# Optimization experiments

Measured on AMD Instinct MI355X. Metric: run time of the kernel, lower is better.

Reference implementation:

```python
import jax, jax.numpy as jnp
import numpy as np

D = 64          # node_hidden_dim
MP_STEPS = 6    # num_step_message_passing
S2S_STEPS = 6   # num_step_set2set
LSTM_LAYERS = 3 # num_layer_set2set


def setup_inputs() -> dict:
    key = jax.random.key(0)
    ks = jax.random.split(key, 32)
    N, E, B = 10000, 50000, 500
    node_in, edge_in, edge_hid, out_dim = 15, 5, 128, 12
    s = 0.1
    inp = {}
    inp["node_feat"] = jax.random.normal(ks[0], (N, node_in), jnp.float32)
    inp["edge_feat"] = jax.random.normal(ks[1], (E, edge_in), jnp.float32)
    inp["src"] = jax.random.randint(ks[2], (E,), 0, N)
    inp["dst"] = jax.random.randint(ks[3], (E,), 0, N)
    inp["graph_ids"] = jnp.sort(jax.random.randint(ks[4], (N,), 0, B))
    inp["num_graphs"] = B
    # lin0
    inp["lin0_W"] = jax.random.normal(ks[5], (node_in, D), jnp.float32) * s
    inp["lin0_b"] = jnp.zeros((D,), jnp.float32)
    # edge network MLP (Linear -> ReLU -> Linear), output reshaped to D x D per edge
    inp["em_W1"] = jax.random.normal(ks[6], (edge_in, edge_hid), jnp.float32) * s
    inp["em_b1"] = jnp.zeros((edge_hid,), jnp.float32)
    inp["em_W2"] = jax.random.normal(ks[7], (edge_hid, D * D), jnp.float32) * 0.02
    inp["em_b2"] = jnp.zeros((D * D,), jnp.float32)
    inp["conv_bias"] = jnp.zeros((D,), jnp.float32)
    # GRU (input D, hidden D), torch layout: [3*D, in], gate order r,z,n
    inp["gru_Wih"] = jax.random.normal(ks[8], (3 * D, D), jnp.float32) * s
    inp["gru_Whh"] = jax.random.normal(ks[9], (3 * D, D), jnp.float32) * s
    inp["gru_bih"] = jnp.zeros((3 * D,), jnp.float32)
    inp["gru_bhh"] = jnp.zeros((3 * D,), jnp.float32)
    # Set2Set LSTM: input 2*D, hidden D, 3 layers. torch layout [4*D, in], gates i,f,g,o
    inp["lstm0_Wih"] = jax.random.normal(ks[10], (4 * D, 2 * D), jnp.float32) * s
    inp["lstm0_Whh"] = jax.random.normal(ks[11], (4 * D, D), jnp.float32) * s
    inp["lstm0_bih"] = jnp.zeros((4 * D,), jnp.float32)
    inp["lstm0_bhh"] = jnp.zeros((4 * D,), jnp.float32)
    inp["lstm12_Wih"] = jax.random.normal(ks[12], (2, 4 * D, D), jnp.float32) * s
    inp["lstm12_Whh"] = jax.random.normal(ks[13], (2, 4 * D, D), jnp.float32) * s
    inp["lstm12_bih"] = jnp.zeros((2, 4 * D), jnp.float32)
    inp["lstm12_bhh"] = jnp.zeros((2, 4 * D), jnp.float32)
    # output head
    inp["lin1_W"] = jax.random.normal(ks[14], (2 * D, D), jnp.float32) * s
    inp["lin1_b"] = jnp.zeros((D,), jnp.float32)
    inp["lin2_W"] = jax.random.normal(ks[15], (D, out_dim), jnp.float32) * s
    inp["lin2_b"] = jnp.zeros((out_dim,), jnp.float32)
    return inp


def _mpnn(node_feat, edge_feat, src, dst, graph_ids, num_graphs,
          lin0_W, lin0_b, em_W1, em_b1, em_W2, em_b2, conv_bias,
          gru_Wih, gru_Whh, gru_bih, gru_bhh,
          lstm0_Wih, lstm0_Whh, lstm0_bih, lstm0_bhh,
          lstm12_Wih, lstm12_Whh, lstm12_bih, lstm12_bhh,
          lin1_W, lin1_b, lin2_W, lin2_b):
    N = node_feat.shape[0]
    E = edge_feat.shape[0]
    B = num_graphs
    # initial node embedding
    out = jax.nn.relu(node_feat @ lin0_W + lin0_b)      # [N, D]
    h = out                                             # GRU hidden (seq_len=1, 1 layer)
    # per-edge weight matrices (edge features are static across steps)
    We = (jax.nn.relu(edge_feat @ em_W1 + em_b1) @ em_W2 + em_b2).reshape(E, D, D)
    for _ in range(MP_STEPS):
        # NNConv: gather src -> per-edge matvec -> scatter-add to dst
        msg = jnp.einsum('ei,eio->eo', out[src], We)    # [E, D]
        agg = jax.ops.segment_sum(msg, dst, num_segments=N) + conv_bias
        m = jax.nn.relu(agg)                            # [N, D]
        # GRU cell (torch gate order r, z, n)
        gx = m @ gru_Wih.T + gru_bih
        gh = h @ gru_Whh.T + gru_bhh
        rx, zx, nx = jnp.split(gx, 3, axis=-1)
        rh, zh, nh = jnp.split(gh, 3, axis=-1)
        r = jax.nn.sigmoid(rx + rh)
        z = jax.nn.sigmoid(zx + zh)
        n = jnp.tanh(nx + r * nh)
        h = (1.0 - z) * n + z * h
        out = h
    # Set2Set readout: 3-layer LSTM over steps, attention over nodes per graph
    h_l = [jnp.zeros((B, D), out.dtype) for _ in range(LSTM_LAYERS)]
    c_l = [jnp.zeros((B, D), out.dtype) for _ in range(LSTM_LAYERS)]
    q_star = jnp.zeros((B, 2 * D), out.dtype)
    for _ in range(S2S_STEPS):
        x = q_star
        for l in range(LSTM_LAYERS):
            if l == 0:
                Wih, Whh, bih, bhh = lstm0_Wih, lstm0_Whh, lstm0_bih, lstm0_bhh
            else:
                Wih, Whh = lstm12_Wih[l - 1], lstm12_Whh[l - 1]
                bih, bhh = lstm12_bih[l - 1], lstm12_bhh[l - 1]
            g = x @ Wih.T + bih + h_l[l] @ Whh.T + bhh
            i_g, f_g, g_g, o_g = jnp.split(g, 4, axis=-1)
            c_l[l] = jax.nn.sigmoid(f_g) * c_l[l] + jax.nn.sigmoid(i_g) * jnp.tanh(g_g)
            h_l[l] = jax.nn.sigmoid(o_g) * jnp.tanh(c_l[l])
            x = h_l[l]
        q = x                                           # [B, D]
        # segment softmax attention
        e = jnp.sum(out * q[graph_ids], axis=-1)        # [N]
        emax = jax.ops.segment_max(e, graph_ids, num_segments=B)
        ex = jnp.exp(e - emax[graph_ids])
        denom = jax.ops.segment_sum(ex, graph_ids, num_segments=B)
        alpha = ex / denom[graph_ids]                   # [N]
        readout = jax.ops.segment_sum(alpha[:, None] * out, graph_ids, num_segments=B)
        q_star = jnp.concatenate([q, readout], axis=-1) # [B, 2D]
    y = jax.nn.relu(q_star @ lin1_W + lin1_b) @ lin2_W + lin2_b
    return y


def reference(node_feat, edge_feat, src, dst, graph_ids, num_graphs,
              lin0_W, lin0_b, em_W1, em_b1, em_W2, em_b2, conv_bias,
              gru_Wih, gru_Whh, gru_bih, gru_bhh,
              lstm0_Wih, lstm0_Whh, lstm0_bih, lstm0_bhh,
              lstm12_Wih, lstm12_Whh, lstm12_bih, lstm12_bhh,
              lin1_W, lin1_b, lin2_W, lin2_b):
    return _mpnn(node_feat, edge_feat, src, dst, graph_ids, num_graphs,
                 lin0_W, lin0_b, em_W1, em_b1, em_W2, em_b2, conv_bias,
                 gru_Wih, gru_Whh, gru_bih, gru_bhh,
                 lstm0_Wih, lstm0_Whh, lstm0_bih, lstm0_bhh,
                 lstm12_Wih, lstm12_Whh, lstm12_bih, lstm12_bhh,
                 lin1_W, lin1_b, lin2_W, lin2_b)
```

## Files before the change

### kernel.cpp

```cpp
#include <hip/hip_runtime.h>
#include <math.h>

#define NGRAPH 500
#define MP_STEPS 6
#define S2S_STEPS 6
#define S2S_CAP 64

typedef _Float16 h8 __attribute__((ext_vector_type(8)));
typedef float f4 __attribute__((ext_vector_type(4)));

__device__ __forceinline__ float sigmoidf_(float v){ return 1.0f/(1.0f + expf(-v)); }

__global__ void k_zero(float* __restrict__ p, int n){
  int i = blockIdx.x*256 + threadIdx.x;
  if(i < n) p[i] = 0.f;
}

__global__ void k_lin0(const float* __restrict__ nf, const float* __restrict__ W,
                       const float* __restrict__ b, float* __restrict__ x, int N){
  int n = blockIdx.x*4 + (threadIdx.x >> 6);
  int d = threadIdx.x & 63;
  if(n >= N) return;
  float acc = b[d];
#pragma unroll
  for(int i=0;i<15;i++) acc = fmaf(nf[n*15+i], W[i*64+d], acc);
  x[n*64+d] = fmaxf(acc, 0.0f);
}

__global__ void k_edgeh(const float* __restrict__ ef, const float* __restrict__ W1,
                        const float* __restrict__ b1, _Float16* __restrict__ he, int E){
  int e = blockIdx.x;
  int h = threadIdx.x;
  if(e >= E) return;
  float acc = b1[h];
#pragma unroll
  for(int i=0;i<5;i++) acc = fmaf(ef[e*5+i], W1[i*128+h], acc);
  he[(size_t)e*128 + h] = (_Float16)fmaxf(acc, 0.f);
}

__global__ void k_prepW2(const float* __restrict__ W2, _Float16* __restrict__ W2T){
  int idx = blockIdx.x*256 + threadIdx.x;
  if(idx >= 4096*128) return;
  int n = idx >> 7, k = idx & 127;
  W2T[idx] = (_Float16)W2[(size_t)k*4096 + n];
}

__global__ __launch_bounds__(512, 4) void k_fmsg(
    const _Float16* __restrict__ he,
    const _Float16* __restrict__ W2T,
    const float* __restrict__ b2,
    const float* __restrict__ x,
    const int* __restrict__ src, const int* __restrict__ dst,
    float* __restrict__ agg, int E)
{
  __shared__ _Float16 hs[128*128];
  __shared__ float xsT[64*128];
  __shared__ int ds_dst[128];
  const int tid  = threadIdx.x;
  const int wave = tid >> 6;
  const int mrow = wave >> 2;
  const int cg   = wave & 3;
  const int lane = tid & 63;
  const int quad = lane >> 4;
  const int l15  = lane & 15;
  const int e0   = blockIdx.x * 128;

  for(int t = tid; t < 2048; t += 512){
    int r = t >> 4, c = t & 15;
    uint4 v = make_uint4(0,0,0,0);
    if(e0 + r < E) v = *(const uint4*)&he[(size_t)(e0+r)*128 + c*8];
    *(uint4*)&hs[r*128 + ((c ^ (r&7)) << 3)] = v;
  }
  {
    int j = tid >> 2, qc = tid & 3;
    int sj = (e0 + j < E) ? src[e0 + j] : 0;
    const float4* xr = (const float4*)(x + (size_t)sj*64);
#pragma unroll
    for(int k=0;k<4;k++){
      float4 v = xr[qc*4 + k];
      int ib = qc*16 + k*4;
      xsT[(ib+0)*128 + j] = v.x;
      xsT[(ib+1)*128 + j] = v.y;
      xsT[(ib+2)*128 + j] = v.z;
      xsT[(ib+3)*128 + j] = v.w;
    }
  }
  if(tid < 128) ds_dst[tid] = (e0 + tid < E) ? dst[e0 + tid] : 0;
  __syncthreads();

  const int l7 = l15 & 7;
  const int qp = quad ^ (l7 & 3);
  const int hp = l7 >> 2;
  const int oA = ((hp << 2) | qp) << 4;
  const int oB = (((1 ^ hp) << 2) | qp) << 4;
  unsigned a0 = (unsigned)((mrow*64 + l15) << 8) + oA;
  unsigned a1 = (unsigned)((mrow*64 + l15) << 8) + oB;
  const char* hsb = (const char*)hs;

  const int col = cg*16 + l15;
  const _Float16* bbase = W2T + ((size_t)col)*128 + (quad<<3);
  h8 bf[4], bn[4];
#pragma unroll
  for(int ks=0;ks<4;ks++) bf[ks] = *(const h8*)(bbase + ks*32);
  float b2f = b2[col], b2n = 0.f;

  f4 macc[4];
#pragma unroll
  for(int mt=0;mt<4;mt++) macc[mt] = (f4){0.f,0.f,0.f,0.f};

#pragma unroll 2
  for(int i=0;i<64;i++){
    if(i < 63){
      const _Float16* nb = bbase + (size_t)(i+1)*8192;
#pragma unroll
      for(int ks=0;ks<4;ks++) bn[ks] = *(const h8*)(nb + ks*32);
      b2n = b2[(i+1)*64 + col];
    }
    f4 g0 = (f4){0.f,0.f,0.f,0.f}, g1 = g0, g2 = g0, g3 = g0;
#pragma unroll
    for(int mt=0;mt<4;mt++){
      h8 A0 = *(const h8*)(hsb + a0 + mt*4096);
      h8 A1 = *(const h8*)(hsb + a1 + mt*4096);
      h8 A2 = *(const h8*)(hsb + a0 + mt*4096 + 128);
      h8 A3 = *(const h8*)(hsb + a1 + mt*4096 + 128);
      f4* g = (mt==0)?&g0:(mt==1)?&g1:(mt==2)?&g2:&g3;
      *g = __builtin_amdgcn_mfma_f32_16x16x32_f16(A0, bf[0], *g, 0, 0, 0);
      *g = __builtin_amdgcn_mfma_f32_16x16x32_f16(A1, bf[1], *g, 0, 0, 0);
      *g = __builtin_amdgcn_mfma_f32_16x16x32_f16(A2, bf[2], *g, 0, 0, 0);
      *g = __builtin_amdgcn_mfma_f32_16x16x32_f16(A3, bf[3], *g, 0, 0, 0);
    }
    g0 += b2f; g1 += b2f; g2 += b2f; g3 += b2f;
    f4 xs0 = *(const f4*)&xsT[i*128 + mrow*64 +  0 + (quad<<2)];
    f4 xs1 = *(const f4*)&xsT[i*128 + mrow*64 + 16 + (quad<<2)];
    f4 xs2 = *(const f4*)&xsT[i*128 + mrow*64 + 32 + (quad<<2)];
    f4 xs3 = *(const f4*)&xsT[i*128 + mrow*64 + 48 + (quad<<2)];
    macc[0] += xs0 * g0;
    macc[1] += xs1 * g1;
    macc[2] += xs2 * g2;
    macc[3] += xs3 * g3;
#pragma unroll
    for(int ks=0;ks<4;ks++) bf[ks] = bn[ks];
    b2f = b2n;
    asm volatile("" : "+v"(a0), "+v"(a1));
  }

#pragma unroll
  for(int mt=0;mt<4;mt++){
#pragma unroll
    for(int r=0;r<4;r++){
      int edge = mrow*64 + mt*16 + (quad<<2) + r;
      if(e0 + edge < E)
        atomicAdd(&agg[(size_t)ds_dst[edge]*64 + col], macc[mt][r]);
    }
  }
}

__global__ __launch_bounds__(256) void k_gru2(
    float* __restrict__ x, float* __restrict__ agg, const float* __restrict__ cb,
    const float* __restrict__ WihT, const float* __restrict__ WhhT,
    const float* __restrict__ bih, const float* __restrict__ bhh, int N)
{
  __shared__ float ms[32*64], hs2[32*64];
  const int tid = threadIdx.x;
  const int n0 = blockIdx.x*32;
  for(int t=tid; t<2048; t+=256){
    int n = n0 + (t>>6), d = t&63;
    float mv=0.f, hv=0.f;
    if(n < N){
      mv = fmaxf(agg[(size_t)n*64+d] + cb[d], 0.f);
      agg[(size_t)n*64+d] = 0.f;
      hv = x[(size_t)n*64+d];
    }
    ms[t]=mv; hs2[t]=hv;
  }
  __syncthreads();
  const int gx = tid & 31, ng = tid >> 5;
  float ar[4][2]={{0}}, az[4][2]={{0}}, anx[4][2]={{0}}, anh[4][2]={{0}};
#pragma unroll 4
  for(int k=0;k<64;k++){
    float wi0=WihT[k*192+gx],     wi1=WihT[k*192+gx+32];
    float wi2=WihT[k*192+gx+64],  wi3=WihT[k*192+gx+96];
    float wi4=WihT[k*192+gx+128], wi5=WihT[k*192+gx+160];
    float wh0=WhhT[k*192+gx],     wh1=WhhT[k*192+gx+32];
    float wh2=WhhT[k*192+gx+64],  wh3=WhhT[k*192+gx+96];
    float wh4=WhhT[k*192+gx+128], wh5=WhhT[k*192+gx+160];
#pragma unroll
    for(int j=0;j<4;j++){
      float mk = ms[(ng*4+j)*64+k], hk = hs2[(ng*4+j)*64+k];
      ar[j][0] = fmaf(mk,wi0, fmaf(hk,wh0, ar[j][0]));
      ar[j][1] = fmaf(mk,wi1, fmaf(hk,wh1, ar[j][1]));
      az[j][0] = fmaf(mk,wi2, fmaf(hk,wh2, az[j][0]));
      az[j][1] = fmaf(mk,wi3, fmaf(hk,wh3, az[j][1]));
      anx[j][0]= fmaf(mk,wi4, anx[j][0]);
      anx[j][1]= fmaf(mk,wi5, anx[j][1]);
      anh[j][0]= fmaf(hk,wh4, anh[j][0]);
      anh[j][1]= fmaf(hk,wh5, anh[j][1]);
    }
  }
#pragma unroll
  for(int j=0;j<4;j++){
    int n = n0 + ng*4 + j;
    if(n >= N) continue;
#pragma unroll
    for(int c=0;c<2;c++){
      int d = gx + 32*c;
      float r  = sigmoidf_(ar[j][c] + bih[d]     + bhh[d]);
      float z  = sigmoidf_(az[j][c] + bih[64+d]  + bhh[64+d]);
      float nn = tanhf(anx[j][c] + bih[128+d] + r*(anh[j][c] + bhh[128+d]));
      float hv = hs2[(ng*4+j)*64+d];
      x[(size_t)n*64+d] = (1.f - z)*nn + z*hv;
    }
  }
}

__global__ void k_tr_gru(const float* __restrict__ Wih, const float* __restrict__ Whh,
                         float* __restrict__ WihT, float* __restrict__ WhhT){
  int idx = blockIdx.x*256 + threadIdx.x;
  if(idx < 192*64){
    int r = idx/64, i = idx%64;
    WihT[i*192 + r] = Wih[idx];
    WhhT[i*192 + r] = Whh[idx];
  }
}

__global__ void k_tr_lstmcat(const float* __restrict__ w0ih, const float* __restrict__ w0hh,
                             const float* __restrict__ w12ih, const float* __restrict__ w12hh,
                             float* __restrict__ W0cat, float* __restrict__ W12cat){
  int idx = blockIdx.x*256 + threadIdx.x;
  if(idx < 192*256){
    int k = idx / 256, r = idx % 256;
    W0cat[idx] = (k < 128) ? w0ih[r*128 + k] : w0hh[r*64 + (k - 128)];
  }
  if(idx < 2*128*256){
    int l = idx / (128*256);
    int rem = idx % (128*256);
    int k = rem / 256, r = rem % 256;
    W12cat[idx] = (k < 64) ? w12ih[((size_t)l*256 + r)*64 + k]
                           : w12hh[((size_t)l*256 + r)*64 + (k - 64)];
  }
}

__device__ __forceinline__ int lbound(const int* __restrict__ a, int n, int v){
  int lo=0, hi=n;
  while(lo<hi){ int mid=(lo+hi)>>1; if(a[mid]<v) lo=mid+1; else hi=mid; }
  return lo;
}

template<int KTOT>
__device__ __forceinline__ void lstm_layer4(
    float (*__restrict__ qcat)[320], float (*__restrict__ csl)[192],
    int xoff, int hoff, int coff,
    const float* __restrict__ Wcat, const float* __restrict__ bsum,
    f4 (*__restrict__ ps4)[256], int t)
{
  constexpr int CH = KTOT/4;
  const int kc = t >> 6, tq = t & 63;
  const float* wp = Wcat + (size_t)(kc*CH)*256 + 4*tq;
  f4 a0 = (f4){0.f,0.f,0.f,0.f}, a1 = a0, a2 = a0, a3 = a0;
#pragma unroll
  for(int i=0;i<CH;i++){
    f4 w = *(const f4*)(wp + (size_t)i*256);
    int xi = xoff + kc*CH + i;
    a0 += qcat[0][xi] * w;
    a1 += qcat[1][xi] * w;
    a2 += qcat[2][xi] * w;
    a3 += qcat[3][xi] * w;
  }
  ps4[0][t] = a0; ps4[1][t] = a1; ps4[2][t] = a2; ps4[3][t] = a3;
  __syncthreads();
  {
    const int g = t >> 6, d = t & 63;
    float v[4];
#pragma unroll
    for(int gate=0; gate<4; gate++){
      int G = gate*64 + d;
      int q = G >> 2, cmp = G & 3;
      float s = 0.f;
#pragma unroll
      for(int k2=0;k2<4;k2++) s += ps4[g][k2*64 + q][cmp];
      v[gate] = s + bsum[G];
    }
    float ig = sigmoidf_(v[0]);
    float fg = sigmoidf_(v[1]);
    float gg = tanhf(v[2]);
    float og = sigmoidf_(v[3]);
    float cn = fg*csl[g][coff+d] + ig*gg;
    csl[g][coff+d] = cn;
    qcat[g][hoff+d] = og*tanhf(cn);
  }
  __syncthreads();
}

__global__ __launch_bounds__(256) void k_s2s(
    const float* __restrict__ x, const int* __restrict__ gid, int N,
    const float* __restrict__ W0cat, const float* __restrict__ W12cat,
    const float* __restrict__ l0_bih, const float* __restrict__ l0_bhh,
    const float* __restrict__ l12_bih, const float* __restrict__ l12_bhh,
    const float* __restrict__ W1, const float* __restrict__ b1,
    const float* __restrict__ W2, const float* __restrict__ b2,
    float* __restrict__ y)
{
  const int b0 = blockIdx.x * 4;
  const int t = threadIdx.x;
  const int wave = t >> 6, lane = t & 63;
  __shared__ float xt[4][S2S_CAP*65];
  __shared__ float qcat[4][320];
  __shared__ float csl[4][192];
  __shared__ f4    ps4[4][256];
  __shared__ float bsum[768];
  __shared__ int   sh_n0[5];

  if(t < 5) sh_n0[t] = lbound(gid, N, b0 + t);
  for(int i=t; i<4*320; i+=256) ((float*)qcat)[i] = 0.f;
  for(int i=t; i<4*192; i+=256) ((float*)csl)[i] = 0.f;
  for(int i=t; i<768; i+=256){
    int layer = i >> 8, g = i & 255;
    float bi, bh;
    if(layer == 0){ bi = l0_bih[g]; bh = l0_bhh[g]; }
    else { bi = l12_bih[(layer-1)*256+g]; bh = l12_bhh[(layer-1)*256+g]; }
    bsum[i] = bi + bh;
  }
  __syncthreads();
  const int n0w = sh_n0[wave];
  const int cntw = sh_n0[wave+1] - n0w;
  const int ccw = (cntw < S2S_CAP) ? cntw : S2S_CAP;

  for(int j=0;j<ccw;j++)
    xt[wave][j*65 + lane] = x[(size_t)(n0w+j)*64 + lane];
  __syncthreads();

  for(int step=0; step<S2S_STEPS; step++){
    lstm_layer4<192>(qcat, csl,   0, 128,   0, W0cat,          bsum,     ps4, t);
    lstm_layer4<128>(qcat, csl, 128, 192,  64, W12cat,         bsum+256, ps4, t);
    lstm_layer4<128>(qcat, csl, 192, 256, 128, W12cat+128*256, bsum+512, ps4, t);

    const float* q = qcat[wave] + 256;
    float accd = 0.f;
    if(lane < ccw){
      const float* xr = xt[wave] + lane*65;
#pragma unroll 8
      for(int k=0;k<64;k++) accd = fmaf(xr[k], q[k], accd);
    }
    float pm = (lane < ccw) ? accd : -1e30f;
    float qv = q[lane];
    for(int j = S2S_CAP; j < cntw; j++){
      float p = x[(size_t)(n0w+j)*64 + lane] * qv;
#pragma unroll
      for(int o=32;o;o>>=1) p += __shfl_xor(p, o, 64);
      pm = fmaxf(pm, p);
    }
#pragma unroll
    for(int o=32;o;o>>=1) pm = fmaxf(pm, __shfl_xor(pm, o, 64));
    const float mx = pm;

    float ex = (lane < ccw) ? expf(accd - mx) : 0.f;
    float exsum = ex;
#pragma unroll
    for(int o=32;o;o>>=1) exsum += __shfl_xor(exsum, o, 64);

    float racc = 0.f;
    for(int j=0;j<ccw;j++)
      racc = fmaf(__shfl(ex, j, 64), xt[wave][j*65 + lane], racc);
    for(int j = S2S_CAP; j < cntw; j++){
      float xv = x[(size_t)(n0w+j)*64 + lane];
      float p = xv * qv;
#pragma unroll
      for(int o=32;o;o>>=1) p += __shfl_xor(p, o, 64);
      float e2 = expf(p - mx);
      exsum += e2;
      racc = fmaf(e2, xv, racc);
    }
    float inv = (exsum > 0.f) ? 1.f/exsum : 0.f;
    qcat[wave][lane]      = qcat[wave][256 + lane];
    qcat[wave][64 + lane] = racc * inv;
    __syncthreads();
  }
  float* hh = (float*)ps4;
  {
    const int g = t >> 6, d = t & 63;
    float a = b1[d];
#pragma unroll 4
    for(int k=0;k<128;k++) a = fmaf(qcat[g][k], W1[k*64+d], a);
    hh[g*64 + d] = fmaxf(a, 0.f);
  }
  __syncthreads();
  if(t < 48){
    int g = t / 12, o = t % 12;
    float out = b2[o];
#pragma unroll 4
    for(int k=0;k<64;k++) out = fmaf(hh[g*64 + k], W2[k*12+o], out);
    y[(size_t)(b0+g)*12 + o] = out;
  }
}

extern "C" void kernel_launch(void* const* d_in, const int* in_sizes, int n_in,
                              void* d_out, int out_size, void* d_ws, size_t ws_size,
                              hipStream_t stream) {
  const float* node_feat = (const float*)d_in[0];
  const float* edge_feat = (const float*)d_in[1];
  const int*   src       = (const int*)d_in[2];
  const int*   dst       = (const int*)d_in[3];
  const int*   gid       = (const int*)d_in[4];
  const float* lin0_W = (const float*)d_in[6];
  const float* lin0_b = (const float*)d_in[7];
  const float* em_W1  = (const float*)d_in[8];
  const float* em_b1  = (const float*)d_in[9];
  const float* em_W2  = (const float*)d_in[10];
  const float* em_b2  = (const float*)d_in[11];
  const float* conv_b = (const float*)d_in[12];
  const float* gru_Wih = (const float*)d_in[13];
  const float* gru_Whh = (const float*)d_in[14];
  const float* gru_bih = (const float*)d_in[15];
  const float* gru_bhh = (const float*)d_in[16];
  const float* l0_Wih = (const float*)d_in[17];
  const float* l0_Whh = (const float*)d_in[18];
  const float* l0_bih = (const float*)d_in[19];
  const float* l0_bhh = (const float*)d_in[20];
  const float* l12_Wih = (const float*)d_in[21];
  const float* l12_Whh = (const float*)d_in[22];
  const float* l12_bih = (const float*)d_in[23];
  const float* l12_bhh = (const float*)d_in[24];
  const float* lin1_W = (const float*)d_in[25];
  const float* lin1_b = (const float*)d_in[26];
  const float* lin2_W = (const float*)d_in[27];
  const float* lin2_b = (const float*)d_in[28];
  float* y = (float*)d_out;

  const int N = in_sizes[0] / 15;
  const int E = in_sizes[1] / 5;
  const int B = NGRAPH;

  char* p = (char*)d_ws;
  auto carve = [&](size_t bytes)->char* {
    char* r = p; p += (bytes + 255) & ~(size_t)255; return r;
  };
  _Float16* he_h = (_Float16*)carve((size_t)E*128*2);
  _Float16* W2T  = (_Float16*)carve((size_t)4096*128*2);
  float* x      = (float*)carve((size_t)N*64*4);
  float* agg    = (float*)carve((size_t)N*64*4);
  float* gWihT  = (float*)carve(192*64*4);
  float* gWhhT  = (float*)carve(192*64*4);
  float* W0cat  = (float*)carve(192*256*4);
  float* W12cat = (float*)carve(2*128*256*4);
  (void)ws_size; (void)n_in; (void)out_size;

  k_lin0<<<(N+3)/4, 256, 0, stream>>>(node_feat, lin0_W, lin0_b, x, N);
  k_edgeh<<<E, 128, 0, stream>>>(edge_feat, em_W1, em_b1, he_h, E);
  k_prepW2<<<(4096*128+255)/256, 256, 0, stream>>>(em_W2, W2T);
  k_tr_gru<<<(192*64+255)/256, 256, 0, stream>>>(gru_Wih, gru_Whh, gWihT, gWhhT);
  k_tr_lstmcat<<<(2*128*256+255)/256, 256, 0, stream>>>(l0_Wih, l0_Whh, l12_Wih, l12_Whh,
                                                        W0cat, W12cat);
  k_zero<<<(N*64+255)/256, 256, 0, stream>>>(agg, N*64);

  const int nblk = (E + 127) / 128;
  for(int s=0; s<MP_STEPS; s++){
    k_fmsg<<<nblk, 512, 0, stream>>>(he_h, W2T, em_b2, x, src, dst, agg, E);
    k_gru2<<<(N+31)/32, 256, 0, stream>>>(x, agg, conv_b, gWihT, gWhhT, gru_bih, gru_bhh, N);
  }

  k_s2s<<<B/4, 256, 0, stream>>>(x, gid, N,
                                 W0cat, W12cat, l0_bih, l0_bhh,
                                 l12_bih, l12_bhh,
                                 lin1_W, lin1_b, lin2_W, lin2_b, y);
}
```

Measured before the change: 1.082 ms.

## Hold A fragments in registers across loop and pad shared arrays

```diff
diff --git a/kernel.cpp b/kernel.cpp
--- a/kernel.cpp
+++ b/kernel.cpp
@@ -45,7 +45,7 @@
   W2T[idx] = (_Float16)W2[(size_t)k*4096 + n];
 }
 
-__global__ __launch_bounds__(512, 4) void k_fmsg(
+__global__ __launch_bounds__(512, 2) void k_fmsg(
     const _Float16* __restrict__ he,
     const _Float16* __restrict__ W2T,
     const float* __restrict__ b2,
@@ -53,8 +53,8 @@
     const int* __restrict__ src, const int* __restrict__ dst,
     float* __restrict__ agg, int E)
 {
-  __shared__ _Float16 hs[128*128];
-  __shared__ float xsT[64*128];
+  __shared__ _Float16 hs[128*136];
+  __shared__ float xsT[64*132];
   __shared__ int ds_dst[128];
   const int tid  = threadIdx.x;
   const int wave = tid >> 6;
@@ -69,7 +69,7 @@
     int r = t >> 4, c = t & 15;
     uint4 v = make_uint4(0,0,0,0);
     if(e0 + r < E) v = *(const uint4*)&he[(size_t)(e0+r)*128 + c*8];
-    *(uint4*)&hs[r*128 + ((c ^ (r&7)) << 3)] = v;
+    *(uint4*)&hs[r*136 + c*8] = v;
   }
   {
     int j = tid >> 2, qc = tid & 3;
@@ -79,23 +79,21 @@
     for(int k=0;k<4;k++){
       float4 v = xr[qc*4 + k];
       int ib = qc*16 + k*4;
-      xsT[(ib+0)*128 + j] = v.x;
-      xsT[(ib+1)*128 + j] = v.y;
-      xsT[(ib+2)*128 + j] = v.z;
-      xsT[(ib+3)*128 + j] = v.w;
+      xsT[(ib+0)*132 + j] = v.x;
+      xsT[(ib+1)*132 + j] = v.y;
+      xsT[(ib+2)*132 + j] = v.z;
+      xsT[(ib+3)*132 + j] = v.w;
     }
   }
   if(tid < 128) ds_dst[tid] = (e0 + tid < E) ? dst[e0 + tid] : 0;
   __syncthreads();
 
-  const int l7 = l15 & 7;
-  const int qp = quad ^ (l7 & 3);
-  const int hp = l7 >> 2;
-  const int oA = ((hp << 2) | qp) << 4;
-  const int oB = (((1 ^ hp) << 2) | qp) << 4;
-  unsigned a0 = (unsigned)((mrow*64 + l15) << 8) + oA;
-  unsigned a1 = (unsigned)((mrow*64 + l15) << 8) + oB;
-  const char* hsb = (const char*)hs;
+  h8 af[4][4];
+#pragma unroll
+  for(int mt=0;mt<4;mt++)
+#pragma unroll
+    for(int ks=0;ks<4;ks++)
+      af[mt][ks] = *(const h8*)&hs[(mrow*64 + mt*16 + l15)*136 + ks*32 + (quad<<3)];
 
   const int col = cg*16 + l15;
   const _Float16* bbase = W2T + ((size_t)col)*128 + (quad<<3);
@@ -118,22 +116,17 @@
     }
     f4 g0 = (f4){0.f,0.f,0.f,0.f}, g1 = g0, g2 = g0, g3 = g0;
 #pragma unroll
-    for(int mt=0;mt<4;mt++){
-      h8 A0 = *(const h8*)(hsb + a0 + mt*4096);
-      h8 A1 = *(const h8*)(hsb + a1 + mt*4096);
-      h8 A2 = *(const h8*)(hsb + a0 + mt*4096 + 128);
-      h8 A3 = *(const h8*)(hsb + a1 + mt*4096 + 128);
-      f4* g = (mt==0)?&g0:(mt==1)?&g1:(mt==2)?&g2:&g3;
-      *g = __builtin_amdgcn_mfma_f32_16x16x32_f16(A0, bf[0], *g, 0, 0, 0);
-      *g = __builtin_amdgcn_mfma_f32_16x16x32_f16(A1, bf[1], *g, 0, 0, 0);
-      *g = __builtin_amdgcn_mfma_f32_16x16x32_f16(A2, bf[2], *g, 0, 0, 0);
-      *g = __builtin_amdgcn_mfma_f32_16x16x32_f16(A3, bf[3], *g, 0, 0, 0);
+    for(int ks=0;ks<4;ks++){
+      g0 = __builtin_amdgcn_mfma_f32_16x16x32_f16(af[0][ks], bf[ks], g0, 0, 0, 0);
+      g1 = __builtin_amdgcn_mfma_f32_16x16x32_f16(af[1][ks], bf[ks], g1, 0, 0, 0);
+      g2 = __builtin_amdgcn_mfma_f32_16x16x32_f16(af[2][ks], bf[ks], g2, 0, 0, 0);
+      g3 = __builtin_amdgcn_mfma_f32_16x16x32_f16(af[3][ks], bf[ks], g3, 0, 0, 0);
     }
     g0 += b2f; g1 += b2f; g2 += b2f; g3 += b2f;
-    f4 xs0 = *(const f4*)&xsT[i*128 + mrow*64 +  0 + (quad<<2)];
-    f4 xs1 = *(const f4*)&xsT[i*128 + mrow*64 + 16 + (quad<<2)];
-    f4 xs2 = *(const f4*)&xsT[i*128 + mrow*64 + 32 + (quad<<2)];
-    f4 xs3 = *(const f4*)&xsT[i*128 + mrow*64 + 48 + (quad<<2)];
+    f4 xs0 = *(const f4*)&xsT[i*132 + mrow*64 + (quad<<2) +  0];
+    f4 xs1 = *(const f4*)&xsT[i*132 + mrow*64 + (quad<<2) + 16];
+    f4 xs2 = *(const f4*)&xsT[i*132 + mrow*64 + (quad<<2) + 32];
+    f4 xs3 = *(const f4*)&xsT[i*132 + mrow*64 + (quad<<2) + 48];
     macc[0] += xs0 * g0;
     macc[1] += xs1 * g1;
     macc[2] += xs2 * g2;
@@ -141,7 +134,6 @@
 #pragma unroll
     for(int ks=0;ks<4;ks++) bf[ks] = bn[ks];
     b2f = b2n;
-    asm volatile("" : "+v"(a0), "+v"(a1));
   }
 
 #pragma unroll
```

After: 1.123 ms. 1.04x slower.
